# Optimization experiments

Measured on AMD Instinct MI355X. Metric: run time of the kernel, lower is better.

## Reference

```python
import jax, jax.numpy as jnp
import numpy as np

N_USERS = 100000
N_ITEMS = 200000
N = N_USERS + N_ITEMS
E = 1200000
D = 64
HEADS = 4
GCN_LAYERS = 2


def setup_inputs() -> dict:
    key = jax.random.key(0)
    ks = jax.random.split(key, 10)
    s = 1.0 / np.sqrt(D)
    return {
        "uEmbeds": jax.random.normal(ks[0], (N_USERS, D), jnp.float32) * s,
        "iEmbeds": jax.random.normal(ks[1], (N_ITEMS, D), jnp.float32) * s,
        "qTrans": jax.random.normal(ks[2], (D, D), jnp.float32) * s,
        "kTrans": jax.random.normal(ks[3], (D, D), jnp.float32) * s,
        "vTrans": jax.random.normal(ks[4], (D, D), jnp.float32) * s,
        "enc_vals": jax.random.uniform(ks[5], (E,), jnp.float32),
        "enc_rows": jax.random.randint(ks[6], (E,), 0, N, jnp.int32),
        "enc_cols": jax.random.randint(ks[7], (E,), 0, N, jnp.int32),
        "dec_rows": jax.random.randint(ks[8], (E,), 0, N, jnp.int32),
        "dec_cols": jax.random.randint(ks[9], (E,), 0, N, jnp.int32),
    }


def _gcn(vals, rows, cols, embeds):
    # spmm: out[r] += vals[e] * embeds[cols[e]]
    msg = vals[:, None] * embeds[cols]  # [E, D]
    return jax.ops.segment_sum(msg, rows, num_segments=N)


def _gt(rows, cols, qT, kT, vT, embeds):
    dh = D // HEADS
    rowE = embeds[rows]  # [E, D]
    colE = embeds[cols]  # [E, D]
    q = (rowE @ qT).reshape(-1, HEADS, dh)
    k = (colE @ kT).reshape(-1, HEADS, dh)
    v = (colE @ vT).reshape(-1, HEADS, dh)
    att = jnp.clip(jnp.einsum('ehd,ehd->eh', q, k), -10.0, 10.0)
    expAtt = jnp.exp(att)  # [E, H]
    attNorm = jax.ops.segment_sum(expAtt, rows, num_segments=N)[rows]
    a = expAtt / (attNorm + 1e-8)
    res = (a[..., None] * v).reshape(-1, D)  # [E, D]
    return jax.ops.segment_sum(res, rows, num_segments=N)


def reference(uEmbeds, iEmbeds, qTrans, kTrans, vTrans,
              enc_vals, enc_rows, enc_cols, dec_rows, dec_cols):
    embeds = jnp.concatenate([uEmbeds, iEmbeds], axis=0)  # [N, D]
    embedsLst = [embeds]
    for _ in range(GCN_LAYERS):
        embedsLst.append(_gcn(enc_vals, enc_rows, enc_cols, embedsLst[-1]))
    embedsLst.append(_gt(dec_rows, dec_cols, qTrans, kTrans, vTrans, embedsLst[-1]))
    out = embedsLst[0]
    for e in embedsLst[1:]:
        out = out + e
    return out[:N_USERS], out[N_USERS:]
```

## Files before the change

### kernel.cpp

```cpp
#include <hip/hip_runtime.h>
#include <math.h>

#define N_USERS 100000
#define NTOT    300000
#define NEDGE   1200000
#define DIM     64

#define NPBS    256
#define BROWS2  1172
#define CAPS    5376
#define SCHUNK  4096
#define NCH     ((NEDGE + SCHUNK - 1) / SCHUNK)
#define PAD5    1280

typedef unsigned short ushort_t;
typedef unsigned int uint_t;

__device__ __forceinline__ float bf2f(ushort_t u) {
    return __uint_as_float(((uint_t)u) << 16);
}
__device__ __forceinline__ ushort_t f2bf(float x) {
    uint_t b = __float_as_uint(x);
    b += 0x7FFFu + ((b >> 16) & 1u);
    return (ushort_t)(b >> 16);
}


__global__ __launch_bounds__(256) void convert_emb0(
    const float* __restrict__ uE, const float* __restrict__ iE,
    ushort_t* __restrict__ emb0b) {
    int i = blockIdx.x * 256 + threadIdx.x;
    if (i >= NTOT * 16) return;
    float4 x = (i < N_USERS * 16) ? reinterpret_cast<const float4*>(uE)[i]
                                  : reinterpret_cast<const float4*>(iE)[i - N_USERS * 16];
    ushort4 o;
    o.x = f2bf(x.x); o.y = f2bf(x.y); o.z = f2bf(x.z); o.w = f2bf(x.w);
    reinterpret_cast<ushort4*>(emb0b)[i] = o;
}

__global__ void init_gcur(int* __restrict__ gE, int* __restrict__ gD) {
    int t = threadIdx.x;
    gE[t] = t * CAPS;
    gD[t] = t * CAPS;
}

__global__ __launch_bounds__(256) void bucket_stage(
    const int* __restrict__ enc_rows, const int* __restrict__ enc_cols,
    const float* __restrict__ enc_vals, const int* __restrict__ dec_rows,
    const int* __restrict__ dec_cols, int* __restrict__ gcurE,
    int* __restrict__ gcurD, int2* __restrict__ stE, int* __restrict__ stD) {
    __shared__ int cnt[NPBS];
    __shared__ int base[NPBS];
    __shared__ int run[NPBS];
    int t = threadIdx.x;
    bool enc = blockIdx.x < NCH;
    int cb = (enc ? blockIdx.x : blockIdx.x - NCH) * SCHUNK;
    int ce = min(cb + SCHUNK, NEDGE);
    const int* rows = enc ? enc_rows : dec_rows;
    cnt[t] = 0; run[t] = 0;
    __syncthreads();
    for (int i = cb + t; i < ce; i += 256) atomicAdd(&cnt[rows[i] / BROWS2], 1);
    __syncthreads();
    base[t] = atomicAdd(enc ? &gcurE[t] : &gcurD[t], cnt[t]);
    __syncthreads();
    if (enc) {
        for (int i = cb + t; i < ce; i += 256) {
            int r = rows[i];
            int p = r / BROWS2;
            int off = atomicAdd(&run[p], 1);
            int2 v;
            v.x = ((r - p * BROWS2) << 19) | enc_cols[i];
            v.y = __float_as_int(enc_vals[i]);
            stE[base[p] + off] = v;
        }
    } else {
        for (int i = cb + t; i < ce; i += 256) {
            int r = rows[i];
            int p = r / BROWS2;
            int off = atomicAdd(&run[p], 1);
            stD[base[p] + off] = ((r - p * BROWS2) << 19) | dec_cols[i];
        }
    }
}

__global__ __launch_bounds__(256) void scanB(
    const int* __restrict__ gcurE, const int* __restrict__ gcurD,
    int* __restrict__ bbE, int* __restrict__ bbD,
    int* __restrict__ rsE, int* __restrict__ rsD) {
    __shared__ int sh[256];
    int t = threadIdx.x;
    int c = gcurE[t] - t * CAPS;
    sh[t] = c; __syncthreads();
    for (int off = 1; off < 256; off <<= 1) {
        int x = (t >= off) ? sh[t - off] : 0; __syncthreads();
        sh[t] += x; __syncthreads();
    }
    bbE[t] = sh[t] - c;
    __syncthreads();
    int cd = gcurD[t] - t * CAPS;
    sh[t] = cd; __syncthreads();
    for (int off = 1; off < 256; off <<= 1) {
        int x = (t >= off) ? sh[t - off] : 0; __syncthreads();
        sh[t] += x; __syncthreads();
    }
    bbD[t] = sh[t] - cd;
    if (t == 0) { rsE[NTOT] = NEDGE; rsD[NTOT] = NEDGE; }
}

__global__ __launch_bounds__(256) void sort_b(
    const int* __restrict__ gcurE, const int* __restrict__ gcurD,
    const int* __restrict__ bbE, const int* __restrict__ bbD,
    const int2* __restrict__ stE, const int* __restrict__ stD,
    int2* __restrict__ penc, int* __restrict__ pdec,
    int* __restrict__ rsE, int* __restrict__ rsD) {
    __shared__ int cnt[PAD5];
    __shared__ int rowst[PAD5];
    __shared__ int tsum[256];
    __shared__ int2 outb[CAPS];
    int t = threadIdx.x;
    bool enc = blockIdx.x < NPBS;
    int b = enc ? blockIdx.x : blockIdx.x - NPBS;
    int rowbase = b * BROWS2;
    int s = b * CAPS;
    int e = enc ? gcurE[b] : gcurD[b];
    int gbase = enc ? bbE[b] : bbD[b];
    int n = e - s;

    for (int i = t; i < PAD5; i += 256) cnt[i] = 0;
    __syncthreads();
    if (enc) {
        for (int i = s + t; i < e; i += 256)
            atomicAdd(&cnt[((uint_t)stE[i].x) >> 19], 1);
    } else {
        for (int i = s + t; i < e; i += 256)
            atomicAdd(&cnt[((uint_t)stD[i]) >> 19], 1);
    }
    __syncthreads();
    int b5 = t * 5, sum = 0;
#pragma unroll
    for (int k = 0; k < 5; ++k) { int c = cnt[b5 + k]; rowst[b5 + k] = sum; sum += c; }
    tsum[t] = sum; __syncthreads();
    for (int off = 1; off < 256; off <<= 1) {
        int x = (t >= off) ? tsum[t - off] : 0; __syncthreads();
        tsum[t] += x; __syncthreads();
    }
    int excl = tsum[t] - sum;
#pragma unroll
    for (int k = 0; k < 5; ++k) {
        rowst[b5 + k] += excl;
        cnt[b5 + k] = rowst[b5 + k];
    }
    __syncthreads();

    if (enc) {
        for (int i = s + t; i < e; i += 256) {
            int2 v = stE[i];
            int lr = ((uint_t)v.x) >> 19;
            int pos = atomicAdd(&cnt[lr], 1);
            outb[pos] = make_int2(v.x & 0x7FFFF, v.y);
        }
        __syncthreads();
        for (int i = t; i < n; i += 256) penc[gbase + i] = outb[i];
        int nrows = min(BROWS2, NTOT - rowbase);
        for (int j = t; j < nrows; j += 256) rsE[rowbase + j] = gbase + rowst[j];
    } else {
        int* ob = (int*)outb;
        for (int i = s + t; i < e; i += 256) {
            int v = stD[i];
            int pos = atomicAdd(&cnt[((uint_t)v) >> 19], 1);
            ob[pos] = v & 0x7FFFF;
        }
        __syncthreads();
        for (int i = t; i < n; i += 256) pdec[gbase + i] = ob[i];
        int nrows = min(BROWS2, NTOT - rowbase);
        for (int j = t; j < nrows; j += 256) rsD[rowbase + j] = gbase + rowst[j];
    }
}

__global__ __launch_bounds__(256) void gcn_gather1(
    const int* __restrict__ rsE, const int2* __restrict__ penc,
    const ushort_t* __restrict__ emb0b, ushort_t* __restrict__ emb1b) {
    int t = blockIdx.x * 256 + threadIdx.x;
    int row = t >> 4, l = t & 15;
    if (row >= NTOT) return;
    int s = rsE[row], e = rsE[row + 1];
    float4 acc = {0.f, 0.f, 0.f, 0.f};
    for (int j = s; j < e; ++j) {
        int2 cv = penc[j];
        float v = __int_as_float(cv.y);
        ushort4 xb = reinterpret_cast<const ushort4*>(emb0b + (size_t)cv.x * DIM)[l];
        acc.x += v * bf2f(xb.x); acc.y += v * bf2f(xb.y);
        acc.z += v * bf2f(xb.z); acc.w += v * bf2f(xb.w);
    }
    ushort4 o;
    o.x = f2bf(acc.x); o.y = f2bf(acc.y); o.z = f2bf(acc.z); o.w = f2bf(acc.w);
    reinterpret_cast<ushort4*>(emb1b)[(size_t)row * 16 + l] = o;
}

__global__ __launch_bounds__(256) void gcn_gather2(
    const int* __restrict__ rsE, const int2* __restrict__ penc,
    const ushort_t* __restrict__ emb1b, const float* __restrict__ uE,
    const float* __restrict__ iE, float* __restrict__ emb2,
    float* __restrict__ out) {
    int t = blockIdx.x * 256 + threadIdx.x;
    int row = t >> 4, l = t & 15;
    if (row >= NTOT) return;
    int s = rsE[row], e = rsE[row + 1];
    float4 acc = {0.f, 0.f, 0.f, 0.f};
    for (int j = s; j < e; ++j) {
        int2 cv = penc[j];
        float v = __int_as_float(cv.y);
        ushort4 xb = reinterpret_cast<const ushort4*>(emb1b + (size_t)cv.x * DIM)[l];
        acc.x += v * bf2f(xb.x); acc.y += v * bf2f(xb.y);
        acc.z += v * bf2f(xb.z); acc.w += v * bf2f(xb.w);
    }
    const float* e0p = (row < N_USERS) ? uE + (size_t)row * DIM
                                       : iE + (size_t)(row - N_USERS) * DIM;
    float4 e0 = reinterpret_cast<const float4*>(e0p)[l];
    ushort4 e1b = reinterpret_cast<const ushort4*>(emb1b)[(size_t)row * 16 + l];
    reinterpret_cast<float4*>(emb2)[(size_t)row * 16 + l] = acc;
    float4 o;
    o.x = e0.x + bf2f(e1b.x) + acc.x; o.y = e0.y + bf2f(e1b.y) + acc.y;
    o.z = e0.z + bf2f(e1b.z) + acc.z; o.w = e0.w + bf2f(e1b.w) + acc.w;
    reinterpret_cast<float4*>(out)[(size_t)row * 16 + l] = o;
}

__global__ __launch_bounds__(256) void qkv_kernel(
    float* __restrict__ emb2, const float* __restrict__ qT,
    const float* __restrict__ kT, const float* __restrict__ vT,
    ushort_t* __restrict__ KV) {
    __shared__ float lds[4 * 4096];
    float* a_t = lds;
    float* bq = lds + 4096;
    float* bk = lds + 8192;
    float* bv = lds + 12288;
    int t = threadIdx.x;
    int R0 = blockIdx.x * 64;

    {
        const float4* q4 = reinterpret_cast<const float4*>(qT);
        const float4* k4 = reinterpret_cast<const float4*>(kT);
        const float4* v4 = reinterpret_cast<const float4*>(vT);
        float4* lq = reinterpret_cast<float4*>(bq);
        float4* lk = reinterpret_cast<float4*>(bk);
        float4* lv = reinterpret_cast<float4*>(bv);
#pragma unroll
        for (int k = 0; k < 4; ++k) {
            lq[t + k * 256] = q4[t + k * 256];
            lk[t + k * 256] = k4[t + k * 256];
            lv[t + k * 256] = v4[t + k * 256];
        }
    }
    {
        int r = t >> 2, qt = t & 3;
        int grow = R0 + r;
        const float4* src = reinterpret_cast<const float4*>(emb2 + (size_t)grow * DIM);
        bool ok = (grow < NTOT);
#pragma unroll
        for (int k = 0; k < 4; ++k) {
            float4 x;
            if (ok) x = src[qt * 4 + k];
            else { x.x = x.y = x.z = x.w = 0.f; }
            int i0 = qt * 16 + k * 4;
            a_t[(i0 + 0) * 64 + r] = x.x;
            a_t[(i0 + 1) * 64 + r] = x.y;
            a_t[(i0 + 2) * 64 + r] = x.z;
            a_t[(i0 + 3) * 64 + r] = x.w;
        }
    }
    __syncthreads();

    int ty = t >> 4, tx = t & 15;
    float cq[4][4] = {}, ck[4][4] = {}, cv[4][4] = {};
#pragma unroll 4
    for (int i = 0; i < 64; ++i) {
        float4 a = *reinterpret_cast<const float4*>(&a_t[i * 64 + ty * 4]);
        float4 q = *reinterpret_cast<const float4*>(&bq[i * 64 + tx * 4]);
        float4 k = *reinterpret_cast<const float4*>(&bk[i * 64 + tx * 4]);
        float4 v = *reinterpret_cast<const float4*>(&bv[i * 64 + tx * 4]);
        float av[4] = {a.x, a.y, a.z, a.w};
        float qv[4] = {q.x, q.y, q.z, q.w};
        float kv[4] = {k.x, k.y, k.z, k.w};
        float vv[4] = {v.x, v.y, v.z, v.w};
#pragma unroll
        for (int r = 0; r < 4; ++r) {
#pragma unroll
            for (int c = 0; c < 4; ++c) {
                cq[r][c] += av[r] * qv[c];
                ck[r][c] += av[r] * kv[c];
                cv[r][c] += av[r] * vv[c];
            }
        }
    }
    __syncthreads();

#pragma unroll
    for (int r = 0; r < 4; ++r) {
        int grow = R0 + ty * 4 + r;
        if (grow >= NTOT) continue;
        float4 sq;
        sq.x = cq[r][0]; sq.y = cq[r][1]; sq.z = cq[r][2]; sq.w = cq[r][3];
        ushort4 skb, svb;
        skb.x = f2bf(ck[r][0]); skb.y = f2bf(ck[r][1]);
        skb.z = f2bf(ck[r][2]); skb.w = f2bf(ck[r][3]);
        svb.x = f2bf(cv[r][0]); svb.y = f2bf(cv[r][1]);
        svb.z = f2bf(cv[r][2]); svb.w = f2bf(cv[r][3]);
        reinterpret_cast<float4*>(emb2 + (size_t)grow * DIM)[tx] = sq;
        reinterpret_cast<ushort4*>(KV + (size_t)grow * 128)[tx] = skb;
        reinterpret_cast<ushort4*>(KV + (size_t)grow * 128)[16 + tx] = svb;
    }
}

__global__ __launch_bounds__(256) void gt_fused(
    const int* __restrict__ rsD, const int* __restrict__ pdec,
    const float* __restrict__ Q, const ushort_t* __restrict__ KV,
    float* __restrict__ out) {
    int t = blockIdx.x * 256 + threadIdx.x;
    int row = t >> 4, l = t & 15;
    if (row >= NTOT) return;
    int s = rsD[row], e = rsD[row + 1];
    float4 q = reinterpret_cast<const float4*>(Q)[(size_t)row * 16 + l];
    float norm = 0.f;
    float4 acc = {0.f, 0.f, 0.f, 0.f};
    for (int j = s; j < e; ++j) {
        int c = pdec[j];
        const ushort_t* kvrow = KV + (size_t)c * 128;
        ushort4 kb = reinterpret_cast<const ushort4*>(kvrow)[l];
        ushort4 vb = reinterpret_cast<const ushort4*>(kvrow)[16 + l];
        float p = q.x * bf2f(kb.x) + q.y * bf2f(kb.y)
                + q.z * bf2f(kb.z) + q.w * bf2f(kb.w);
        p += __shfl_xor(p, 1);
        p += __shfl_xor(p, 2);
        p = fminf(10.f, fmaxf(-10.f, p));
        float ex = __expf(p);
        norm += ex;
        acc.x += ex * bf2f(vb.x); acc.y += ex * bf2f(vb.y);
        acc.z += ex * bf2f(vb.z); acc.w += ex * bf2f(vb.w);
    }
    float inv = 1.f / (norm + 1e-8f);
    float4 o = reinterpret_cast<float4*>(out)[(size_t)row * 16 + l];
    o.x += acc.x * inv; o.y += acc.y * inv;
    o.z += acc.z * inv; o.w += acc.w * inv;
    reinterpret_cast<float4*>(out)[(size_t)row * 16 + l] = o;
}

extern "C" void kernel_launch(void* const* d_in, const int* in_sizes, int n_in,
                              void* d_out, int out_size, void* d_ws, size_t ws_size,
                              hipStream_t stream) {
    const float* uE       = (const float*)d_in[0];
    const float* iE       = (const float*)d_in[1];
    const float* qT       = (const float*)d_in[2];
    const float* kT       = (const float*)d_in[3];
    const float* vT       = (const float*)d_in[4];
    const float* enc_vals = (const float*)d_in[5];
    const int*   enc_rows = (const int*)d_in[6];
    const int*   enc_cols = (const int*)d_in[7];
    const int*   dec_rows = (const int*)d_in[8];
    const int*   dec_cols = (const int*)d_in[9];
    float* out = (float*)d_out;

    const size_t ND = (size_t)NTOT * DIM;
    float*    ws    = (float*)d_ws;
    float*    emb2  = ws;
    ushort_t* emb0b = (ushort_t*)(ws + ND);
    ushort_t* emb1b = emb0b + ND;
    ushort_t* KV    = emb1b + ND;
    int*      rsE   = (int*)(KV + 2 * ND);
    int*      rsD   = rsE + NTOT + 1;
    int2*     penc  = (int2*)(rsD + NTOT + 1);
    int*      pdec  = (int*)(penc + NEDGE);
    int*      gcurE = pdec + NEDGE;
    int*      gcurD = gcurE + NPBS;
    int*      bbE   = gcurD + NPBS;
    int*      bbD   = bbE + NPBS;

    int2*     stE   = (int2*)KV;
    int*      stD   = (int*)(stE + (size_t)NPBS * CAPS);

    const int GB  = (NTOT * 16) / 256;
    const int QB  = (NTOT + 63) / 64;

    init_gcur<<<1, 256, 0, stream>>>(gcurE, gcurD);
    convert_emb0<<<GB, 256, 0, stream>>>(uE, iE, emb0b);

    bucket_stage<<<2 * NCH, 256, 0, stream>>>(enc_rows, enc_cols, enc_vals,
                                              dec_rows, dec_cols, gcurE, gcurD, stE, stD);
    scanB<<<1, 256, 0, stream>>>(gcurE, gcurD, bbE, bbD, rsE, rsD);
    sort_b<<<2 * NPBS, 256, 0, stream>>>(gcurE, gcurD, bbE, bbD, stE, stD,
                                         penc, pdec, rsE, rsD);

    gcn_gather1<<<GB, 256, 0, stream>>>(rsE, penc, emb0b, emb1b);
    gcn_gather2<<<GB, 256, 0, stream>>>(rsE, penc, emb1b, uE, iE, emb2, out);

    qkv_kernel<<<QB, 256, 0, stream>>>(emb2, qT, kT, vT, KV);
    gt_fused<<<GB, 256, 0, stream>>>(rsD, pdec, emb2, KV, out);
}
```

Measured before the change: 438.5 us.

## Compute QKV projection with bf16 MFMA instead of FP32 LDS tiled GEMM

Replaces the FP32 shared-memory QKV GEMM with a wavefront-level bf16 MFMA kernel. The QKV weights are pre-transposed to bf16 in a small prep kernel, and emb2 is now stored as bf16 rather than fp32, which halves that write and the read that follows. Q is written as fp32 into the reused emb0b workspace. The output stores are scalar and strided per column, which may coalesce worse than the old vectorized stores. Rounding emb2 to bf16 before the projection adds precision loss.

After: 409.7 us. -6.6%, faster.

```diff
diff --git a/kernel.cpp b/kernel.cpp
--- a/kernel.cpp
+++ b/kernel.cpp
@@ -15,6 +15,8 @@
 
 typedef unsigned short ushort_t;
 typedef unsigned int uint_t;
+typedef __attribute__((ext_vector_type(8))) short short8;
+typedef __attribute__((ext_vector_type(4))) float f32x4;
 
 __device__ __forceinline__ float bf2f(ushort_t u) {
     return __uint_as_float(((uint_t)u) << 16);
@@ -36,6 +38,17 @@
     ushort4 o;
     o.x = f2bf(x.x); o.y = f2bf(x.y); o.z = f2bf(x.z); o.w = f2bf(x.w);
     reinterpret_cast<ushort4*>(emb0b)[i] = o;
+}
+
+__global__ void bt_prep(const float* __restrict__ qT, const float* __restrict__ kT,
+                        const float* __restrict__ vT, ushort_t* __restrict__ Bt) {
+    int t = threadIdx.x;
+    for (int idx = t; idx < 4096; idx += 256) {
+        int k = idx >> 6, c = idx & 63;
+        Bt[c * 64 + k]        = f2bf(qT[idx]);
+        Bt[4096 + c * 64 + k] = f2bf(kT[idx]);
+        Bt[8192 + c * 64 + k] = f2bf(vT[idx]);
+    }
 }
 
 __global__ void init_gcur(int* __restrict__ gE, int* __restrict__ gD) {
@@ -200,7 +213,7 @@
 __global__ __launch_bounds__(256) void gcn_gather2(
     const int* __restrict__ rsE, const int2* __restrict__ penc,
     const ushort_t* __restrict__ emb1b, const float* __restrict__ uE,
-    const float* __restrict__ iE, float* __restrict__ emb2,
+    const float* __restrict__ iE, ushort_t* __restrict__ emb2b,
     float* __restrict__ out) {
     int t = blockIdx.x * 256 + threadIdx.x;
     int row = t >> 4, l = t & 15;
@@ -218,96 +231,69 @@
                                        : iE + (size_t)(row - N_USERS) * DIM;
     float4 e0 = reinterpret_cast<const float4*>(e0p)[l];
     ushort4 e1b = reinterpret_cast<const ushort4*>(emb1b)[(size_t)row * 16 + l];
-    reinterpret_cast<float4*>(emb2)[(size_t)row * 16 + l] = acc;
+    ushort4 o2;
+    o2.x = f2bf(acc.x); o2.y = f2bf(acc.y); o2.z = f2bf(acc.z); o2.w = f2bf(acc.w);
+    reinterpret_cast<ushort4*>(emb2b)[(size_t)row * 16 + l] = o2;
     float4 o;
     o.x = e0.x + bf2f(e1b.x) + acc.x; o.y = e0.y + bf2f(e1b.y) + acc.y;
     o.z = e0.z + bf2f(e1b.z) + acc.z; o.w = e0.w + bf2f(e1b.w) + acc.w;
     reinterpret_cast<float4*>(out)[(size_t)row * 16 + l] = o;
 }
 
-__global__ __launch_bounds__(256) void qkv_kernel(
-    float* __restrict__ emb2, const float* __restrict__ qT,
-    const float* __restrict__ kT, const float* __restrict__ vT,
-    ushort_t* __restrict__ KV) {
-    __shared__ float lds[4 * 4096];
-    float* a_t = lds;
-    float* bq = lds + 4096;
-    float* bk = lds + 8192;
-    float* bv = lds + 12288;
-    int t = threadIdx.x;
-    int R0 = blockIdx.x * 64;
-
-    {
-        const float4* q4 = reinterpret_cast<const float4*>(qT);
-        const float4* k4 = reinterpret_cast<const float4*>(kT);
-        const float4* v4 = reinterpret_cast<const float4*>(vT);
-        float4* lq = reinterpret_cast<float4*>(bq);
-        float4* lk = reinterpret_cast<float4*>(bk);
-        float4* lv = reinterpret_cast<float4*>(bv);
-#pragma unroll
-        for (int k = 0; k < 4; ++k) {
-            lq[t + k * 256] = q4[t + k * 256];
-            lk[t + k * 256] = k4[t + k * 256];
-            lv[t + k * 256] = v4[t + k * 256];
-        }
-    }
-    {
-        int r = t >> 2, qt = t & 3;
-        int grow = R0 + r;
-        const float4* src = reinterpret_cast<const float4*>(emb2 + (size_t)grow * DIM);
-        bool ok = (grow < NTOT);
-#pragma unroll
-        for (int k = 0; k < 4; ++k) {
-            float4 x;
-            if (ok) x = src[qt * 4 + k];
-            else { x.x = x.y = x.z = x.w = 0.f; }
-            int i0 = qt * 16 + k * 4;
-            a_t[(i0 + 0) * 64 + r] = x.x;
-            a_t[(i0 + 1) * 64 + r] = x.y;
-            a_t[(i0 + 2) * 64 + r] = x.z;
-            a_t[(i0 + 3) * 64 + r] = x.w;
-        }
-    }
-    __syncthreads();
-
-    int ty = t >> 4, tx = t & 15;
-    float cq[4][4] = {}, ck[4][4] = {}, cv[4][4] = {};
-#pragma unroll 4
-    for (int i = 0; i < 64; ++i) {
-        float4 a = *reinterpret_cast<const float4*>(&a_t[i * 64 + ty * 4]);
-        float4 q = *reinterpret_cast<const float4*>(&bq[i * 64 + tx * 4]);
-        float4 k = *reinterpret_cast<const float4*>(&bk[i * 64 + tx * 4]);
-        float4 v = *reinterpret_cast<const float4*>(&bv[i * 64 + tx * 4]);
-        float av[4] = {a.x, a.y, a.z, a.w};
-        float qv[4] = {q.x, q.y, q.z, q.w};
-        float kv[4] = {k.x, k.y, k.z, k.w};
-        float vv[4] = {v.x, v.y, v.z, v.w};
-#pragma unroll
-        for (int r = 0; r < 4; ++r) {
-#pragma unroll
-            for (int c = 0; c < 4; ++c) {
-                cq[r][c] += av[r] * qv[c];
-                ck[r][c] += av[r] * kv[c];
-                cv[r][c] += av[r] * vv[c];
+__global__ __launch_bounds__(256) void qkv_mfma(
+    const ushort_t* __restrict__ emb2b, const ushort_t* __restrict__ Bt,
+    float* __restrict__ Q, ushort_t* __restrict__ KV) {
+    int tid = threadIdx.x;
+    int w = tid >> 6, lane = tid & 63;
+    int lr = lane & 15, lh = lane >> 4;
+    int R0 = blockIdx.x * 256 + w * 64;
+
+    short8 a[4][2];
+    short8 z8 = {0, 0, 0, 0, 0, 0, 0, 0};
+#pragma unroll
+    for (int m = 0; m < 4; ++m) {
+        int row = R0 + m * 16 + lr;
+        if (row < NTOT) {
+            const ushort_t* ap = emb2b + (size_t)row * 64 + lh * 8;
+            a[m][0] = *reinterpret_cast<const short8*>(ap);
+            a[m][1] = *reinterpret_cast<const short8*>(ap + 32);
+        } else {
+            a[m][0] = z8; a[m][1] = z8;
+        }
+    }
+
+#pragma unroll
+    for (int n = 0; n < 4; ++n) {
+        int col = n * 16 + lr;
+        const ushort_t* bp = Bt + (size_t)col * 64 + lh * 8;
+        short8 bq0 = *reinterpret_cast<const short8*>(bp);
+        short8 bq1 = *reinterpret_cast<const short8*>(bp + 32);
+        short8 bk0 = *reinterpret_cast<const short8*>(bp + 4096);
+        short8 bk1 = *reinterpret_cast<const short8*>(bp + 4096 + 32);
+        short8 bv0 = *reinterpret_cast<const short8*>(bp + 8192);
+        short8 bv1 = *reinterpret_cast<const short8*>(bp + 8192 + 32);
+#pragma unroll
+        for (int m = 0; m < 4; ++m) {
+            f32x4 aq = {0.f, 0.f, 0.f, 0.f};
+            f32x4 ak = {0.f, 0.f, 0.f, 0.f};
+            f32x4 av = {0.f, 0.f, 0.f, 0.f};
+            aq = __builtin_amdgcn_mfma_f32_16x16x32_bf16(a[m][0], bq0, aq, 0, 0, 0);
+            aq = __builtin_amdgcn_mfma_f32_16x16x32_bf16(a[m][1], bq1, aq, 0, 0, 0);
+            ak = __builtin_amdgcn_mfma_f32_16x16x32_bf16(a[m][0], bk0, ak, 0, 0, 0);
+            ak = __builtin_amdgcn_mfma_f32_16x16x32_bf16(a[m][1], bk1, ak, 0, 0, 0);
+            av = __builtin_amdgcn_mfma_f32_16x16x32_bf16(a[m][0], bv0, av, 0, 0, 0);
+            av = __builtin_amdgcn_mfma_f32_16x16x32_bf16(a[m][1], bv1, av, 0, 0, 0);
+            int rbase = R0 + m * 16 + lh * 4;
+#pragma unroll
+            for (int r = 0; r < 4; ++r) {
+                int srow = rbase + r;
+                if (srow < NTOT) {
+                    Q[(size_t)srow * 64 + col] = aq[r];
+                    KV[(size_t)srow * 128 + col] = f2bf(ak[r]);
+                    KV[(size_t)srow * 128 + 64 + col] = f2bf(av[r]);
+                }
             }
         }
-    }
-    __syncthreads();
-
-#pragma unroll
-    for (int r = 0; r < 4; ++r) {
-        int grow = R0 + ty * 4 + r;
-        if (grow >= NTOT) continue;
-        float4 sq;
-        sq.x = cq[r][0]; sq.y = cq[r][1]; sq.z = cq[r][2]; sq.w = cq[r][3];
-        ushort4 skb, svb;
-        skb.x = f2bf(ck[r][0]); skb.y = f2bf(ck[r][1]);
-        skb.z = f2bf(ck[r][2]); skb.w = f2bf(ck[r][3]);
-        svb.x = f2bf(cv[r][0]); svb.y = f2bf(cv[r][1]);
-        svb.z = f2bf(cv[r][2]); svb.w = f2bf(cv[r][3]);
-        reinterpret_cast<float4*>(emb2 + (size_t)grow * DIM)[tx] = sq;
-        reinterpret_cast<ushort4*>(KV + (size_t)grow * 128)[tx] = skb;
-        reinterpret_cast<ushort4*>(KV + (size_t)grow * 128)[16 + tx] = svb;
     }
 }
 
@@ -360,12 +346,12 @@
     float* out = (float*)d_out;
 
     const size_t ND = (size_t)NTOT * DIM;
-    float*    ws    = (float*)d_ws;
-    float*    emb2  = ws;
-    ushort_t* emb0b = (ushort_t*)(ws + ND);
+    ushort_t* emb0b = (ushort_t*)d_ws;
     ushort_t* emb1b = emb0b + ND;
-    ushort_t* KV    = emb1b + ND;
-    int*      rsE   = (int*)(KV + 2 * ND);
+    ushort_t* emb2b = emb1b + ND;
+    ushort_t* KV    = emb2b + ND;
+    ushort_t* Bt    = KV + 2 * ND;
+    int*      rsE   = (int*)(Bt + 3 * 4096);
     int*      rsD   = rsE + NTOT + 1;
     int2*     penc  = (int2*)(rsD + NTOT + 1);
     int*      pdec  = (int*)(penc + NEDGE);
@@ -374,14 +360,16 @@
     int*      bbE   = gcurD + NPBS;
     int*      bbD   = bbE + NPBS;
 
+    float*    Q     = (float*)emb0b;
     int2*     stE   = (int2*)KV;
     int*      stD   = (int*)(stE + (size_t)NPBS * CAPS);
 
     const int GB  = (NTOT * 16) / 256;
-    const int QB  = (NTOT + 63) / 64;
+    const int QB  = (NTOT + 255) / 256;
 
     init_gcur<<<1, 256, 0, stream>>>(gcurE, gcurD);
     convert_emb0<<<GB, 256, 0, stream>>>(uE, iE, emb0b);
+    bt_prep<<<1, 256, 0, stream>>>(qT, kT, vT, Bt);
 
     bucket_stage<<<2 * NCH, 256, 0, stream>>>(enc_rows, enc_cols, enc_vals,
                                               dec_rows, dec_cols, gcurE, gcurD, stE, stD);
@@ -390,8 +378,8 @@
                                          penc, pdec, rsE, rsD);
 
     gcn_gather1<<<GB, 256, 0, stream>>>(rsE, penc, emb0b, emb1b);
-    gcn_gather2<<<GB, 256, 0, stream>>>(rsE, penc, emb1b, uE, iE, emb2, out);
-
-    qkv_kernel<<<QB, 256, 0, stream>>>(emb2, qT, kT, vT, KV);
-    gt_fused<<<GB, 256, 0, stream>>>(rsD, pdec, emb2, KV, out);
-}
+    gcn_gather2<<<GB, 256, 0, stream>>>(rsE, penc, emb1b, uE, iE, emb2b, out);
+
+    qkv_mfma<<<QB, 256, 0, stream>>>(emb2b, Bt, Q, KV);
+    gt_fused<<<GB, 256, 0, stream>>>(rsD, pdec, Q, KV, out);
+}
```
